# Kernel optimization log

Hardware: AMD Instinct MI355X
Metric: run time of the kernel (lower is better)

## Reference

```python
import jax, jax.numpy as jnp
import numpy as np

B, M, L, D = 4, 4, 512, 1024
N_HEAD = 16
D_HEAD = D // N_HEAD
LN_EPS = 1e-6


def setup_inputs() -> dict:
    key = jax.random.key(0)
    ks = jax.random.split(key, 9)
    s = 1.0 / np.sqrt(D)
    return {
        "q": jax.random.normal(ks[0], (B, M, L, D), dtype=jnp.float32),
        "k": jax.random.normal(ks[1], (B, M, L, D), dtype=jnp.float32),
        "qi": jax.random.normal(ks[2], (B, M, L, D), dtype=jnp.float32),
        "mask": jax.random.randint(ks[3], (B, M, L, L), 0, 2, dtype=jnp.int32),
        "w_qs": jax.random.normal(ks[4], (D, D), dtype=jnp.float32) * s,
        "w_qis": jax.random.normal(ks[5], (D, D), dtype=jnp.float32) * s,
        "w_fc": jax.random.normal(ks[6], (D, D), dtype=jnp.float32) * s,
        "ln_g": jnp.ones((D,), dtype=jnp.float32),
        "ln_b": jnp.zeros((D,), dtype=jnp.float32),
    }


def _l2_normalize(x):
    # normaliseE: divide by sqrt(sum of squares) over the last axis (no eps)
    return x / jnp.sqrt(jnp.sum(x * x, axis=-1, keepdims=True))


def _softmax2d(attn):
    # softmax jointly over the (doc, key) axes = axes (1, 4) of [B,M,H,Lq,Lk]
    m = jnp.max(attn, axis=(1, 4), keepdims=True)
    e = jnp.exp(attn - m)
    return e / jnp.sum(e, axis=(1, 4), keepdims=True)


def reference(q, k, qi, mask, w_qs, w_qis, w_fc, ln_g, ln_b):
    del k  # unused by the original forward
    b, m, lq, d = q.shape
    residual = q

    # LayerNorm(d_model, eps=1e-6) on q only
    mu = jnp.mean(q, axis=-1, keepdims=True)
    var = jnp.mean(jnp.square(q - mu), axis=-1, keepdims=True)
    qn = (q - mu) / jnp.sqrt(var + LN_EPS) * ln_g + ln_b

    # projections (bias-free) and head split -> [B,M,H,L,d_head]
    qh = (qn @ w_qs).reshape(b, m, lq, N_HEAD, D_HEAD)
    qih = (qi @ w_qis).reshape(b, m, qi.shape[2], N_HEAD, D_HEAD)
    qh = jnp.swapaxes(_l2_normalize(qh), 2, 3)
    qih = jnp.swapaxes(_l2_normalize(qih), 2, 3)

    # cosine-similarity scores (BSM=True -> no temperature scaling)
    attn = jnp.einsum("bmhqd,bmhkd->bmhqk", qh, qih)

    # mask broadcast over heads (the torch transpose dance is equivalent)
    attn = jnp.where(mask[:, :, None, :, :] == 0, -1e9, attn)

    attn = _softmax2d(attn)  # dropout is identity at eval

    out = jnp.einsum("bmhqk,bmhkd->bmhqd", attn, qih)
    out = jnp.swapaxes(out, 2, 3).reshape(b, m, lq, d)
    out = out @ w_fc + residual
    return out, attn
```

## Files before the change

### kernel.cpp

```cpp
#include <hip/hip_runtime.h>
#include <hip/hip_bf16.h>
#include <cstdint>
#include <cstddef>

#define Bq 4
#define Mq 4
#define Lseq 512
#define Dmod 1024
#define Hq 16
#define DHq 64

using bf16 = __bf16;
using bf16x4 = __attribute__((ext_vector_type(4))) __bf16;
using bf16x8 = __attribute__((ext_vector_type(8))) __bf16;
using f32x4 = __attribute__((ext_vector_type(4))) float;

__device__ __forceinline__ void gld_lds16(const bf16* g, bf16* l) {
  __builtin_amdgcn_global_load_lds(
      (const __attribute__((address_space(1))) void*)g,
      (__attribute__((address_space(3))) void*)l, 16, 0, 0);
}

template <int WAVES_M, int WAVES_N, int WTM, int WTN>
__device__ __forceinline__ void gemm_core(const bf16* __restrict__ A,
                                          const bf16* __restrict__ Bt,
                                          int K, int lda, int ldb,
                                          bf16* As, bf16* Bs,
                                          f32x4 (&acc)[WTM][WTN]) {
  constexpr int BM = WAVES_M * WTM * 16;
  constexpr int BN = WAVES_N * WTN * 16;
  constexpr int IA = BM / 64;
  constexpr int IB = BN / 64;

  const int t = threadIdx.x;
  const int lane = t & 63;
  const int wave = t >> 6;
  const int wm = wave % WAVES_M;
  const int wn = wave / WAVES_M;
  const int r = t >> 2;
  const int c8 = (t & 3) * 8;
  const int fr = lane & 15;
  const int fk = (lane >> 4) * 8;

  const bf16* Ab = A + (size_t)r * lda + c8;
  const bf16* Bb = Bt + (size_t)r * ldb + c8;

  for (int k0 = 0; k0 < K; k0 += 32) {
    if (k0) __syncthreads();
#pragma unroll
    for (int i = 0; i < IA; ++i)
      gld_lds16(Ab + (size_t)i * 64 * lda + k0, As + i * 2048 + t * 8);
#pragma unroll
    for (int i = 0; i < IB; ++i)
      gld_lds16(Bb + (size_t)i * 64 * ldb + k0, Bs + i * 2048 + t * 8);
    asm volatile("s_waitcnt vmcnt(0)" ::: "memory");
    __syncthreads();

    bf16x8 af[WTM], bfv[WTN];
#pragma unroll
    for (int i = 0; i < WTM; ++i)
      af[i] = *(const bf16x8*)(As + (wm * WTM * 16 + i * 16 + fr) * 32 + fk);
#pragma unroll
    for (int j = 0; j < WTN; ++j)
      bfv[j] = *(const bf16x8*)(Bs + (wn * WTN * 16 + j * 16 + fr) * 32 + fk);
#pragma unroll
    for (int i = 0; i < WTM; ++i)
#pragma unroll
      for (int j = 0; j < WTN; ++j)
        acc[i][j] = __builtin_amdgcn_mfma_f32_16x16x32_bf16(af[i], bfv[j],
                                                            acc[i][j], 0, 0, 0);
  }
}

__global__ __launch_bounds__(256) void gemm_bt_128_l2n(
    const bf16* __restrict__ A, const bf16* __restrict__ Bt,
    bf16* __restrict__ C, int K, int lda, int ldb, int ldc) {
  __shared__ __align__(16) bf16 As[128 * 32];
  __shared__ __align__(16) bf16 Bs[128 * 32];
  f32x4 acc[4][4] = {};
  const bf16* Ab = A + (size_t)blockIdx.y * 128 * lda;
  const bf16* Bb = Bt + (size_t)blockIdx.x * 128 * ldb;
  gemm_core<2, 2, 4, 4>(Ab, Bb, K, lda, ldb, As, Bs, acc);

  const int t = threadIdx.x, lane = t & 63, wave = t >> 6;
  const int wm = wave & 1, wn = wave >> 1;
  const int cr = (lane >> 4) * 4, cc = lane & 15;
  const size_t row0 = (size_t)blockIdx.y * 128 + wm * 64;
  const size_t col0 = (size_t)blockIdx.x * 128 + wn * 64;
#pragma unroll
  for (int i = 0; i < 4; ++i)
#pragma unroll
    for (int rg = 0; rg < 4; ++rg) {
      float ss = 0.0f;
#pragma unroll
      for (int j = 0; j < 4; ++j) ss += acc[i][j][rg] * acc[i][j][rg];
      ss += __shfl_xor(ss, 1);
      ss += __shfl_xor(ss, 2);
      ss += __shfl_xor(ss, 4);
      ss += __shfl_xor(ss, 8);
      const float r = (ss > 0.0f) ? rsqrtf(ss) : 0.0f;
#pragma unroll
      for (int j = 0; j < 4; ++j)
        C[(row0 + i * 16 + cr + rg) * ldc + col0 + j * 16 + cc] =
            (bf16)(acc[i][j][rg] * r);
    }
}

__global__ __launch_bounds__(256) void gemm_bt_resid(
    const bf16* __restrict__ A, const bf16* __restrict__ Bt,
    const float* __restrict__ resid, float* __restrict__ C, int K, int lda,
    int ldb, int ldc) {
  __shared__ __align__(16) bf16 As[128 * 32];
  __shared__ __align__(16) bf16 Bs[128 * 32];
  f32x4 acc[4][4] = {};
  const bf16* Ab = A + (size_t)blockIdx.y * 128 * lda;
  const bf16* Bb = Bt + (size_t)blockIdx.x * 128 * ldb;
  gemm_core<2, 2, 4, 4>(Ab, Bb, K, lda, ldb, As, Bs, acc);

  const int t = threadIdx.x, lane = t & 63, wave = t >> 6;
  const int wm = wave & 1, wn = wave >> 1;
  const int cr = (lane >> 4) * 4, cc = lane & 15;
  const size_t row0 = (size_t)blockIdx.y * 128 + wm * 64;
  const size_t col0 = (size_t)blockIdx.x * 128 + wn * 64;
#pragma unroll
  for (int i = 0; i < 4; ++i)
#pragma unroll
    for (int j = 0; j < 4; ++j)
#pragma unroll
      for (int rg = 0; rg < 4; ++rg) {
        size_t idx = (row0 + i * 16 + cr + rg) * ldc + col0 + j * 16 + cc;
        float rv = __builtin_nontemporal_load(resid + idx);
        __builtin_nontemporal_store(acc[i][j][rg] + rv, C + idx);
      }
}

__global__ __launch_bounds__(256) void denom_kernel(
    const bf16* __restrict__ qh, const bf16* __restrict__ qih,
    const int* __restrict__ mask, float* __restrict__ denom) {
  __shared__ __align__(16) bf16 Qs[128 * 64];
  __shared__ __align__(16) bf16 Ks[2][64 * 64];

  const int z = blockIdx.y;
  const int bm = z >> 4, h = z & 15;
  const int q0 = blockIdx.x * 128;

  const int t = threadIdx.x;
  const int lane = t & 63;
  const int wave = t >> 6;
  const int wm = wave & 1, wn = wave >> 1;
  const int fr = lane & 15;
  const int hi = lane >> 4;
  const int sr = t >> 3;
  const int sc = t & 7;

  const bf16* qh_b = qh + ((size_t)bm * Lseq + q0) * Dmod + h * DHq;
  const bf16* qih_b = qih + (size_t)bm * Lseq * Dmod + h * DHq;
  const int* mrow = mask + (size_t)bm * Lseq * Lseq;

#pragma unroll
  for (int s = 0; s < 4; ++s) {
    const int r = s * 32 + sr;
    gld_lds16(qh_b + (size_t)r * Dmod + ((sc ^ (r & 7)) << 3),
              Qs + s * 2048 + t * 8);
  }
#pragma unroll
  for (int s = 0; s < 2; ++s) {
    const int r = s * 32 + sr;
    gld_lds16(qih_b + (size_t)r * Dmod + ((sc ^ (r & 7)) << 3),
              Ks[0] + s * 2048 + t * 8);
  }

  float racc[4][4] = {};

  for (int kt = 0; kt < 8; ++kt) {
    asm volatile("s_waitcnt vmcnt(0)" ::: "memory");
    __syncthreads();
    const bf16* Kc = Ks[kt & 1];

    f32x4 acc_s[4][2] = {};
    __builtin_amdgcn_s_setprio(1);
#pragma unroll
    for (int kk = 0; kk < 2; ++kk) {
      bf16x8 bq[4], bk[2];
#pragma unroll
      for (int i = 0; i < 4; ++i) {
        const int row = wm * 64 + i * 16 + fr;
        bq[i] = *(const bf16x8*)(Qs + row * 64 +
                                 ((((kk << 2) + hi) ^ (row & 7)) << 3));
      }
#pragma unroll
      for (int j = 0; j < 2; ++j) {
        const int row = wn * 32 + j * 16 + fr;
        bk[j] = *(const bf16x8*)(Kc + row * 64 +
                                 ((((kk << 2) + hi) ^ (row & 7)) << 3));
      }
#pragma unroll
      for (int i = 0; i < 4; ++i)
#pragma unroll
        for (int j = 0; j < 2; ++j)
          acc_s[i][j] = __builtin_amdgcn_mfma_f32_16x16x32_bf16(
              bq[i], bk[j], acc_s[i][j], 0, 0, 0);
    }
    __builtin_amdgcn_s_setprio(0);

    if (kt < 7) {
      const int kv1 = (kt + 1) * 64;
#pragma unroll
      for (int s = 0; s < 2; ++s) {
        const int r = s * 32 + sr;
        gld_lds16(qih_b + (size_t)(kv1 + r) * Dmod + ((sc ^ (r & 7)) << 3),
                  Ks[(kt + 1) & 1] + s * 2048 + t * 8);
      }
    }

    const int kv0 = kt * 64;
#pragma unroll
    for (int i = 0; i < 4; ++i)
#pragma unroll
      for (int j = 0; j < 2; ++j)
#pragma unroll
        for (int rg = 0; rg < 4; ++rg) {
          const int qg = q0 + wm * 64 + i * 16 + hi * 4 + rg;
          const int cg = kv0 + wn * 32 + j * 16 + fr;
          if (mrow[(size_t)qg * Lseq + cg] != 0)
            racc[i][rg] += __expf(acc_s[i][j][rg] - 1.0f);
        }
  }

  float* dp = denom + ((size_t)(bm >> 2) * Hq + h) * Lseq + q0 + wm * 64;
#pragma unroll
  for (int i = 0; i < 4; ++i)
#pragma unroll
    for (int rg = 0; rg < 4; ++rg) {
      float rs = racc[i][rg];
      rs += __shfl_xor(rs, 1);
      rs += __shfl_xor(rs, 2);
      rs += __shfl_xor(rs, 4);
      rs += __shfl_xor(rs, 8);
      if (fr == 0) atomicAdd(dp + i * 16 + hi * 4 + rg, rs);
    }
}

__global__ __launch_bounds__(256) void fused_attn(
    const bf16* __restrict__ qh, const bf16* __restrict__ qih,
    const bf16* __restrict__ qih_t, const int* __restrict__ mask,
    const float* __restrict__ denom, float* __restrict__ attn,
    bf16* __restrict__ outh) {
  __shared__ __align__(16) bf16 Qs[128 * 64];
  __shared__ __align__(16) bf16 Ks[64 * 64];
  __shared__ __align__(16) bf16 Vs[2][64 * 64];
  __shared__ __align__(16) bf16 Ps[128 * 64];

  const int z = blockIdx.y;
  const int bm = z >> 4, h = z & 15;
  const int q0 = blockIdx.x * 128;

  const int t = threadIdx.x;
  const int lane = t & 63;
  const int wave = t >> 6;
  const int wm = wave & 1, wn = wave >> 1;
  const int fr = lane & 15;
  const int hi = lane >> 4;
  const int sr = t >> 3;
  const int sc = t & 7;

  const bf16* qh_b = qh + ((size_t)bm * Lseq + q0) * Dmod + h * DHq;
  const bf16* qih_b = qih + (size_t)bm * Lseq * Dmod + h * DHq;
  const bf16* vt_b = qih_t + (size_t)z * DHq * Lseq;
  const int* mrow = mask + (size_t)bm * Lseq * Lseq;
  float* arow = attn + (size_t)z * Lseq * Lseq;

#pragma unroll
  for (int s = 0; s < 4; ++s) {
    const int r = s * 32 + sr;
    gld_lds16(qh_b + (size_t)r * Dmod + ((sc ^ (r & 7)) << 3),
              Qs + s * 2048 + t * 8);
  }
#pragma unroll
  for (int s = 0; s < 2; ++s) {
    const int r = s * 32 + sr;
    gld_lds16(qih_b + (size_t)r * Dmod + ((sc ^ (r & 7)) << 3),
              Ks + s * 2048 + t * 8);
    gld_lds16(vt_b + (size_t)r * Lseq + ((sc ^ (r & 7)) << 3),
              Vs[0] + s * 2048 + t * 8);
  }

  const float* drow = denom + ((size_t)(bm >> 2) * Hq + h) * Lseq + q0;
  float invd[4][4];
#pragma unroll
  for (int i = 0; i < 4; ++i)
#pragma unroll
    for (int rg = 0; rg < 4; ++rg) {
      const float d = drow[wm * 64 + i * 16 + hi * 4 + rg];
      invd[i][rg] = (d > 0.0f) ? 1.0f / d : 0.0f;
    }

  f32x4 acc_o[4][2] = {};

  for (int kt = 0; kt < 8; ++kt) {
    const int kv0 = kt * 64;
    asm volatile("s_waitcnt vmcnt(0)" ::: "memory");
    __syncthreads();

    f32x4 acc_s[4][2] = {};
    __builtin_amdgcn_s_setprio(1);
#pragma unroll
    for (int kk = 0; kk < 2; ++kk) {
      bf16x8 bq[4], bk[2];
#pragma unroll
      for (int i = 0; i < 4; ++i) {
        const int row = wm * 64 + i * 16 + fr;
        bq[i] = *(const bf16x8*)(Qs + row * 64 +
                                 ((((kk << 2) + hi) ^ (row & 7)) << 3));
      }
#pragma unroll
      for (int j = 0; j < 2; ++j) {
        const int row = wn * 32 + j * 16 + fr;
        bk[j] = *(const bf16x8*)(Ks + row * 64 +
                                 ((((kk << 2) + hi) ^ (row & 7)) << 3));
      }
#pragma unroll
      for (int i = 0; i < 4; ++i)
#pragma unroll
        for (int j = 0; j < 2; ++j)
          acc_s[i][j] = __builtin_amdgcn_mfma_f32_16x16x32_bf16(
              bq[i], bk[j], acc_s[i][j], 0, 0, 0);
    }
    __builtin_amdgcn_s_setprio(0);
    __syncthreads();

    if (kt < 7) {
      const int kv1 = kv0 + 64;
#pragma unroll
      for (int s = 0; s < 2; ++s) {
        const int r = s * 32 + sr;
        gld_lds16(qih_b + (size_t)(kv1 + r) * Dmod + ((sc ^ (r & 7)) << 3),
                  Ks + s * 2048 + t * 8);
        gld_lds16(vt_b + (size_t)r * Lseq + kv1 + ((sc ^ (r & 7)) << 3),
                  Vs[(kt + 1) & 1] + s * 2048 + t * 8);
      }
    }

#pragma unroll
    for (int i = 0; i < 4; ++i)
#pragma unroll
      for (int j = 0; j < 2; ++j)
#pragma unroll
        for (int rg = 0; rg < 4; ++rg) {
          const int ql = wm * 64 + i * 16 + hi * 4 + rg;
          const int cl = wn * 32 + j * 16 + fr;
          const int qg = q0 + ql;
          const int cg = kv0 + cl;
          float p = 0.0f;
          if (mrow[(size_t)qg * Lseq + cg] != 0)
            p = __expf(acc_s[i][j][rg] - 1.0f) * invd[i][rg];
          __builtin_nontemporal_store(p, arow + (size_t)qg * Lseq + cg);
          Ps[ql * 64 + (((cl >> 3) ^ (ql & 7)) << 3) + (cl & 7)] = (bf16)p;
        }
    __syncthreads();

    const bf16* Vc = Vs[kt & 1];
    __builtin_amdgcn_s_setprio(1);
#pragma unroll
    for (int kk = 0; kk < 2; ++kk) {
      bf16x8 ap[4], bv[2];
#pragma unroll
      for (int i = 0; i < 4; ++i) {
        const int row = wm * 64 + i * 16 + fr;
        ap[i] = *(const bf16x8*)(Ps + row * 64 +
                                 ((((kk << 2) + hi) ^ (row & 7)) << 3));
      }
#pragma unroll
      for (int j = 0; j < 2; ++j) {
        const int row = wn * 32 + j * 16 + fr;
        bv[j] = *(const bf16x8*)(Vc + row * 64 +
                                 ((((kk << 2) + hi) ^ (row & 7)) << 3));
      }
#pragma unroll
      for (int i = 0; i < 4; ++i)
#pragma unroll
        for (int j = 0; j < 2; ++j)
          acc_o[i][j] = __builtin_amdgcn_mfma_f32_16x16x32_bf16(
              ap[i], bv[j], acc_o[i][j], 0, 0, 0);
    }
    __builtin_amdgcn_s_setprio(0);
    __syncthreads();
  }

  bf16* Cb = outh + ((size_t)bm * Lseq + q0) * Dmod + h * DHq;
#pragma unroll
  for (int i = 0; i < 4; ++i)
#pragma unroll
    for (int j = 0; j < 2; ++j)
#pragma unroll
      for (int rg = 0; rg < 4; ++rg)
        Cb[(size_t)(wm * 64 + i * 16 + hi * 4 + rg) * Dmod + wn * 32 +
           j * 16 + fr] = (bf16)acc_o[i][j][rg];
}

__global__ __launch_bounds__(256) void ln_kernel(const float* __restrict__ q,
                                                 const float* __restrict__ g,
                                                 const float* __restrict__ b,
                                                 bf16* __restrict__ qn) {
  const size_t row = blockIdx.x;
  const float* x = q + row * Dmod;
  bf16* y = qn + row * Dmod;
  const int t = threadIdx.x;
  float4 v = *(const float4*)(x + t * 4);
  float s = v.x + v.y + v.z + v.w;
  float ss = v.x * v.x + v.y * v.y + v.z * v.z + v.w * v.w;
  for (int off = 32; off; off >>= 1) {
    s += __shfl_xor(s, off);
    ss += __shfl_xor(ss, off);
  }
  __shared__ float sm[8];
  const int wave = t >> 6, lane = t & 63;
  if (lane == 0) { sm[wave * 2] = s; sm[wave * 2 + 1] = ss; }
  __syncthreads();
  s = sm[0] + sm[2] + sm[4] + sm[6];
  ss = sm[1] + sm[3] + sm[5] + sm[7];
  const float mean = s * (1.0f / Dmod);
  const float var = ss * (1.0f / Dmod) - mean * mean;
  const float rstd = rsqrtf(var + 1e-6f);
  float4 gg = *(const float4*)(g + t * 4);
  float4 bb = *(const float4*)(b + t * 4);
  bf16x4 o;
  o[0] = (bf16)((v.x - mean) * rstd * gg.x + bb.x);
  o[1] = (bf16)((v.y - mean) * rstd * gg.y + bb.y);
  o[2] = (bf16)((v.z - mean) * rstd * gg.z + bb.z);
  o[3] = (bf16)((v.w - mean) * rstd * gg.w + bb.w);
  *(bf16x4*)(y + t * 4) = o;
}

__global__ __launch_bounds__(256) void cvt_f32_bf16(const float* __restrict__ in,
                                                    bf16* __restrict__ out) {
  const size_t i = ((size_t)blockIdx.x * 256 + threadIdx.x) * 4;
  float4 v = *(const float4*)(in + i);
  bf16x4 o;
  o[0] = (bf16)v.x; o[1] = (bf16)v.y; o[2] = (bf16)v.z; o[3] = (bf16)v.w;
  *(bf16x4*)(out + i) = o;
}

__global__ __launch_bounds__(256) void transpose64_f32(
    const float* __restrict__ in, bf16* __restrict__ out, int ld_in,
    int ld_out) {
  __shared__ bf16 tile[64 * 65];
  const int r0 = blockIdx.y * 64, c0 = blockIdx.x * 64;
  const int t = threadIdx.x, cl = t & 63, rq = t >> 6;
#pragma unroll
  for (int it = 0; it < 16; ++it) {
    const int rl = it * 4 + rq;
    tile[cl * 65 + rl] = (bf16)in[(size_t)(r0 + rl) * ld_in + c0 + cl];
  }
  __syncthreads();
#pragma unroll
  for (int it = 0; it < 16; ++it) {
    const int ol = it * 4 + rq;
    out[(size_t)(c0 + ol) * ld_out + r0 + cl] = tile[ol * 65 + cl];
  }
}

__global__ __launch_bounds__(256) void transpose_qih(
    const bf16* __restrict__ qih, bf16* __restrict__ qih_t) {
  __shared__ bf16 tile[64 * 65];
  const int z = blockIdx.z;
  const int bm = z >> 4, h = z & 15;
  const bf16* in = qih + (size_t)bm * Lseq * Dmod + h * DHq;
  bf16* out = qih_t + (size_t)z * DHq * Lseq;
  const int r0 = blockIdx.x * 64;
  const int t = threadIdx.x, cl = t & 63, rq = t >> 6;
#pragma unroll
  for (int it = 0; it < 16; ++it) {
    const int rl = it * 4 + rq;
    tile[cl * 65 + rl] = in[(size_t)(r0 + rl) * Dmod + cl];
  }
  __syncthreads();
#pragma unroll
  for (int it = 0; it < 16; ++it) {
    const int dh = it * 4 + rq;
    out[(size_t)dh * Lseq + r0 + cl] = tile[dh * 65 + cl];
  }
}

extern "C" void kernel_launch(void* const* d_in, const int* in_sizes, int n_in,
                              void* d_out, int out_size, void* d_ws,
                              size_t ws_size, hipStream_t stream) {
  const float* q = (const float*)d_in[0];
  const float* qi = (const float*)d_in[2];
  const int* mask = (const int*)d_in[3];
  const float* w_qs = (const float*)d_in[4];
  const float* w_qis = (const float*)d_in[5];
  const float* w_fc = (const float*)d_in[6];
  const float* ln_g = (const float*)d_in[7];
  const float* ln_b = (const float*)d_in[8];

  float* out = (float*)d_out;
  const size_t NE = (size_t)Bq * Mq * Lseq * Dmod;
  float* attn = out + NE;

  char* attnc = (char*)attn;
  bf16* qib = (bf16*)attnc;
  bf16* wqs_t = (bf16*)(attnc + (16u << 20));
  bf16* wqis_t = (bf16*)(attnc + (18u << 20));

  char* ws = (char*)d_ws;
  const size_t SZ = NE * sizeof(bf16);
  bf16* qn = (bf16*)(ws);
  bf16* qh = (bf16*)(ws + SZ);
  bf16* qih = (bf16*)(ws + 2 * SZ);
  bf16* qih_t = (bf16*)(ws + 3 * SZ);
  bf16* wfc_t = (bf16*)(ws + 4 * SZ);
  float* denom = (float*)(ws + 4 * SZ + (2u << 20));
  bf16* outh = qn;

  const int ROWS = Bq * Mq * Lseq;

  cvt_f32_bf16<<<NE / 1024, 256, 0, stream>>>(qi, qib);
  transpose64_f32<<<dim3(16, 16), 256, 0, stream>>>(w_qs, wqs_t, Dmod, Dmod);
  transpose64_f32<<<dim3(16, 16), 256, 0, stream>>>(w_qis, wqis_t, Dmod, Dmod);
  transpose64_f32<<<dim3(16, 16), 256, 0, stream>>>(w_fc, wfc_t, Dmod, Dmod);
  hipMemsetAsync(denom, 0, (size_t)Bq * Hq * Lseq * sizeof(float), stream);

  ln_kernel<<<ROWS, 256, 0, stream>>>(q, ln_g, ln_b, qn);

  gemm_bt_128_l2n<<<dim3(Dmod / 128, ROWS / 128), 256, 0, stream>>>(
      qn, wqs_t, qh, Dmod, Dmod, Dmod, Dmod);
  gemm_bt_128_l2n<<<dim3(Dmod / 128, ROWS / 128), 256, 0, stream>>>(
      qib, wqis_t, qih, Dmod, Dmod, Dmod, Dmod);

  transpose_qih<<<dim3(Lseq / 64, 1, Bq * Mq * Hq), 256, 0, stream>>>(qih,
                                                                      qih_t);

  denom_kernel<<<dim3(Lseq / 128, Bq * Mq * Hq), 256, 0, stream>>>(
      qh, qih, mask, denom);

  fused_attn<<<dim3(Lseq / 128, Bq * Mq * Hq), 256, 0, stream>>>(
      qh, qih, qih_t, mask, denom, attn, outh);

  gemm_bt_resid<<<dim3(Dmod / 128, ROWS / 128), 256, 0, stream>>>(
      outh, wfc_t, q, out, Dmod, Dmod, Dmod, Dmod);
}
```

Measured before the change: 615.6 us.

## Pack mask to bitmasks, double-buffer K/P tiles, and swizzle attention block order

A new pre-pass packs the int32 mask into 64-bit ballot words, so the denominator and fused attention kernels each read one u64 per row per key tile instead of 64 ints. The fused attention kernel now double-buffers K and P in LDS and issues the next tile's loads right after the barrier. That lets it drop two __syncthreads per iteration in favour of a single lgkmcnt wait plus barrier. Blocks are remapped with a swizzle so blocks launched together spread across different (bm,h) slices. These changes add an extra kernel launch and more LDS use per block, which may lower occupancy.

```diff
diff --git a/kernel.cpp b/kernel.cpp
--- a/kernel.cpp
+++ b/kernel.cpp
@@ -14,6 +14,7 @@
 using bf16x4 = __attribute__((ext_vector_type(4))) __bf16;
 using bf16x8 = __attribute__((ext_vector_type(8))) __bf16;
 using f32x4 = __attribute__((ext_vector_type(4))) float;
+using u64 = unsigned long long;
 
 __device__ __forceinline__ void gld_lds16(const bf16* g, bf16* l) {
   __builtin_amdgcn_global_load_lds(
@@ -134,15 +135,33 @@
       }
 }
 
+__global__ __launch_bounds__(256) void mask_to_bits(
+    const int* __restrict__ mask, u64* __restrict__ mb) {
+  const int wid = blockIdx.x * 4 + (threadIdx.x >> 6);
+  const int lane = threadIdx.x & 63;
+#pragma unroll
+  for (int it = 0; it < 16; ++it) {
+    const size_t W = (size_t)wid * 16 + it;
+    const u64 b = __ballot(mask[W * 64 + lane] != 0);
+    if (lane == 0) mb[W] = b;
+  }
+}
+
+__device__ __forceinline__ void attn_swizzle(int flat, int& z, int& q0) {
+  const int slot = flat >> 3;
+  z = (flat & 7) * 32 + (slot >> 2);
+  q0 = (slot & 3) * 128;
+}
+
 __global__ __launch_bounds__(256) void denom_kernel(
     const bf16* __restrict__ qh, const bf16* __restrict__ qih,
-    const int* __restrict__ mask, float* __restrict__ denom) {
+    const u64* __restrict__ mb, float* __restrict__ denom) {
   __shared__ __align__(16) bf16 Qs[128 * 64];
   __shared__ __align__(16) bf16 Ks[2][64 * 64];
 
-  const int z = blockIdx.y;
+  int z, q0;
+  attn_swizzle(blockIdx.x, z, q0);
   const int bm = z >> 4, h = z & 15;
-  const int q0 = blockIdx.x * 128;
 
   const int t = threadIdx.x;
   const int lane = t & 63;
@@ -155,7 +174,7 @@
 
   const bf16* qh_b = qh + ((size_t)bm * Lseq + q0) * Dmod + h * DHq;
   const bf16* qih_b = qih + (size_t)bm * Lseq * Dmod + h * DHq;
-  const int* mrow = mask + (size_t)bm * Lseq * Lseq;
+  const u64* mrow = mb + (size_t)bm * Lseq * 8;
 
 #pragma unroll
   for (int s = 0; s < 4; ++s) {
@@ -175,8 +194,26 @@
   for (int kt = 0; kt < 8; ++kt) {
     asm volatile("s_waitcnt vmcnt(0)" ::: "memory");
     __syncthreads();
+
+    if (kt < 7) {
+      const int kv1 = (kt + 1) * 64;
+#pragma unroll
+      for (int s = 0; s < 2; ++s) {
+        const int r = s * 32 + sr;
+        gld_lds16(qih_b + (size_t)(kv1 + r) * Dmod + ((sc ^ (r & 7)) << 3),
+                  Ks[(kt + 1) & 1] + s * 2048 + t * 8);
+      }
+    }
+
+    u64 mw[4][4];
+#pragma unroll
+    for (int i = 0; i < 4; ++i)
+#pragma unroll
+      for (int rg = 0; rg < 4; ++rg)
+        mw[i][rg] =
+            mrow[(size_t)(q0 + wm * 64 + i * 16 + hi * 4 + rg) * 8 + kt];
+
     const bf16* Kc = Ks[kt & 1];
-
     f32x4 acc_s[4][2] = {};
     __builtin_amdgcn_s_setprio(1);
 #pragma unroll
@@ -203,28 +240,16 @@
     }
     __builtin_amdgcn_s_setprio(0);
 
-    if (kt < 7) {
-      const int kv1 = (kt + 1) * 64;
-#pragma unroll
-      for (int s = 0; s < 2; ++s) {
-        const int r = s * 32 + sr;
-        gld_lds16(qih_b + (size_t)(kv1 + r) * Dmod + ((sc ^ (r & 7)) << 3),
-                  Ks[(kt + 1) & 1] + s * 2048 + t * 8);
-      }
-    }
-
-    const int kv0 = kt * 64;
 #pragma unroll
     for (int i = 0; i < 4; ++i)
 #pragma unroll
-      for (int j = 0; j < 2; ++j)
-#pragma unroll
-        for (int rg = 0; rg < 4; ++rg) {
-          const int qg = q0 + wm * 64 + i * 16 + hi * 4 + rg;
-          const int cg = kv0 + wn * 32 + j * 16 + fr;
-          if (mrow[(size_t)qg * Lseq + cg] != 0)
+      for (int rg = 0; rg < 4; ++rg) {
+        const unsigned hw = (unsigned)(mw[i][rg] >> (wn * 32));
+#pragma unroll
+        for (int j = 0; j < 2; ++j)
+          if ((hw >> (j * 16 + fr)) & 1)
             racc[i][rg] += __expf(acc_s[i][j][rg] - 1.0f);
-        }
+      }
   }
 
   float* dp = denom + ((size_t)(bm >> 2) * Hq + h) * Lseq + q0 + wm * 64;
@@ -243,17 +268,17 @@
 
 __global__ __launch_bounds__(256) void fused_attn(
     const bf16* __restrict__ qh, const bf16* __restrict__ qih,
-    const bf16* __restrict__ qih_t, const int* __restrict__ mask,
+    const bf16* __restrict__ qih_t, const u64* __restrict__ mb,
     const float* __restrict__ denom, float* __restrict__ attn,
     bf16* __restrict__ outh) {
   __shared__ __align__(16) bf16 Qs[128 * 64];
-  __shared__ __align__(16) bf16 Ks[64 * 64];
+  __shared__ __align__(16) bf16 Ks[2][64 * 64];
   __shared__ __align__(16) bf16 Vs[2][64 * 64];
-  __shared__ __align__(16) bf16 Ps[128 * 64];
-
-  const int z = blockIdx.y;
+  __shared__ __align__(16) bf16 Ps[2][128 * 64];
+
+  int z, q0;
+  attn_swizzle(blockIdx.x, z, q0);
   const int bm = z >> 4, h = z & 15;
-  const int q0 = blockIdx.x * 128;
 
   const int t = threadIdx.x;
   const int lane = t & 63;
@@ -267,7 +292,7 @@
   const bf16* qh_b = qh + ((size_t)bm * Lseq + q0) * Dmod + h * DHq;
   const bf16* qih_b = qih + (size_t)bm * Lseq * Dmod + h * DHq;
   const bf16* vt_b = qih_t + (size_t)z * DHq * Lseq;
-  const int* mrow = mask + (size_t)bm * Lseq * Lseq;
+  const u64* mrow = mb + (size_t)bm * Lseq * 8;
   float* arow = attn + (size_t)z * Lseq * Lseq;
 
 #pragma unroll
@@ -280,7 +305,7 @@
   for (int s = 0; s < 2; ++s) {
     const int r = s * 32 + sr;
     gld_lds16(qih_b + (size_t)r * Dmod + ((sc ^ (r & 7)) << 3),
-              Ks + s * 2048 + t * 8);
+              Ks[0] + s * 2048 + t * 8);
     gld_lds16(vt_b + (size_t)r * Lseq + ((sc ^ (r & 7)) << 3),
               Vs[0] + s * 2048 + t * 8);
   }
@@ -302,6 +327,27 @@
     asm volatile("s_waitcnt vmcnt(0)" ::: "memory");
     __syncthreads();
 
+    if (kt < 7) {
+      const int kv1 = kv0 + 64;
+#pragma unroll
+      for (int s = 0; s < 2; ++s) {
+        const int r = s * 32 + sr;
+        gld_lds16(qih_b + (size_t)(kv1 + r) * Dmod + ((sc ^ (r & 7)) << 3),
+                  Ks[(kt + 1) & 1] + s * 2048 + t * 8);
+        gld_lds16(vt_b + (size_t)r * Lseq + kv1 + ((sc ^ (r & 7)) << 3),
+                  Vs[(kt + 1) & 1] + s * 2048 + t * 8);
+      }
+    }
+
+    u64 mw[4][4];
+#pragma unroll
+    for (int i = 0; i < 4; ++i)
+#pragma unroll
+      for (int rg = 0; rg < 4; ++rg)
+        mw[i][rg] =
+            mrow[(size_t)(q0 + wm * 64 + i * 16 + hi * 4 + rg) * 8 + kt];
+
+    const bf16* Kc = Ks[kt & 1];
     f32x4 acc_s[4][2] = {};
     __builtin_amdgcn_s_setprio(1);
 #pragma unroll
@@ -316,7 +362,7 @@
 #pragma unroll
       for (int j = 0; j < 2; ++j) {
         const int row = wn * 32 + j * 16 + fr;
-        bk[j] = *(const bf16x8*)(Ks + row * 64 +
+        bk[j] = *(const bf16x8*)(Kc + row * 64 +
                                  ((((kk << 2) + hi) ^ (row & 7)) << 3));
       }
 #pragma unroll
@@ -327,20 +373,8 @@
               bq[i], bk[j], acc_s[i][j], 0, 0, 0);
     }
     __builtin_amdgcn_s_setprio(0);
-    __syncthreads();
-
-    if (kt < 7) {
-      const int kv1 = kv0 + 64;
-#pragma unroll
-      for (int s = 0; s < 2; ++s) {
-        const int r = s * 32 + sr;
-        gld_lds16(qih_b + (size_t)(kv1 + r) * Dmod + ((sc ^ (r & 7)) << 3),
-                  Ks + s * 2048 + t * 8);
-        gld_lds16(vt_b + (size_t)r * Lseq + kv1 + ((sc ^ (r & 7)) << 3),
-                  Vs[(kt + 1) & 1] + s * 2048 + t * 8);
-      }
-    }
-
+
+    bf16* Pc = Ps[kt & 1];
 #pragma unroll
     for (int i = 0; i < 4; ++i)
 #pragma unroll
@@ -349,15 +383,16 @@
         for (int rg = 0; rg < 4; ++rg) {
           const int ql = wm * 64 + i * 16 + hi * 4 + rg;
           const int cl = wn * 32 + j * 16 + fr;
-          const int qg = q0 + ql;
-          const int cg = kv0 + cl;
+          const unsigned hw = (unsigned)(mw[i][rg] >> (wn * 32));
           float p = 0.0f;
-          if (mrow[(size_t)qg * Lseq + cg] != 0)
+          if ((hw >> (j * 16 + fr)) & 1)
             p = __expf(acc_s[i][j][rg] - 1.0f) * invd[i][rg];
-          __builtin_nontemporal_store(p, arow + (size_t)qg * Lseq + cg);
-          Ps[ql * 64 + (((cl >> 3) ^ (ql & 7)) << 3) + (cl & 7)] = (bf16)p;
+          __builtin_nontemporal_store(
+              p, arow + (size_t)(q0 + ql) * Lseq + kv0 + cl);
+          Pc[ql * 64 + (((cl >> 3) ^ (ql & 7)) << 3) + (cl & 7)] = (bf16)p;
         }
-    __syncthreads();
+    asm volatile("s_waitcnt lgkmcnt(0)" ::: "memory");
+    __builtin_amdgcn_s_barrier();
 
     const bf16* Vc = Vs[kt & 1];
     __builtin_amdgcn_s_setprio(1);
@@ -367,7 +402,7 @@
 #pragma unroll
       for (int i = 0; i < 4; ++i) {
         const int row = wm * 64 + i * 16 + fr;
-        ap[i] = *(const bf16x8*)(Ps + row * 64 +
+        ap[i] = *(const bf16x8*)(Pc + row * 64 +
                                  ((((kk << 2) + hi) ^ (row & 7)) << 3));
       }
 #pragma unroll
@@ -384,7 +419,6 @@
               ap[i], bv[j], acc_o[i][j], 0, 0, 0);
     }
     __builtin_amdgcn_s_setprio(0);
-    __syncthreads();
   }
 
   bf16* Cb = outh + ((size_t)bm * Lseq + q0) * Dmod + h * DHq;
@@ -511,10 +545,12 @@
   bf16* qih_t = (bf16*)(ws + 3 * SZ);
   bf16* wfc_t = (bf16*)(ws + 4 * SZ);
   float* denom = (float*)(ws + 4 * SZ + (2u << 20));
+  u64* mbits = (u64*)(ws + 4 * SZ + (4u << 20));
   bf16* outh = qn;
 
   const int ROWS = Bq * Mq * Lseq;
 
+  mask_to_bits<<<1024, 256, 0, stream>>>(mask, mbits);
   cvt_f32_bf16<<<NE / 1024, 256, 0, stream>>>(qi, qib);
   transpose64_f32<<<dim3(16, 16), 256, 0, stream>>>(w_qs, wqs_t, Dmod, Dmod);
   transpose64_f32<<<dim3(16, 16), 256, 0, stream>>>(w_qis, wqis_t, Dmod, Dmod);
@@ -531,11 +567,10 @@
   transpose_qih<<<dim3(Lseq / 64, 1, Bq * Mq * Hq), 256, 0, stream>>>(qih,
                                                                       qih_t);
 
-  denom_kernel<<<dim3(Lseq / 128, Bq * Mq * Hq), 256, 0, stream>>>(
-      qh, qih, mask, denom);
-
-  fused_attn<<<dim3(Lseq / 128, Bq * Mq * Hq), 256, 0, stream>>>(
-      qh, qih, qih_t, mask, denom, attn, outh);
+  denom_kernel<<<1024, 256, 0, stream>>>(qh, qih, mbits, denom);
+
+  fused_attn<<<1024, 256, 0, stream>>>(qh, qih, qih_t, mbits, denom, attn,
+                                       outh);
 
   gemm_bt_resid<<<dim3(Dmod / 128, ROWS / 128), 256, 0, stream>>>(
       outh, wfc_t, q, out, Dmod, Dmod, Dmod, Dmod);
```

Result: faster. 600.5 us (-2.5%).
